# Kernel optimization log

Hardware: AMD Instinct MI355X
Metric: run time of the kernel (lower is better)

Reference implementation:

```python
import jax, jax.numpy as jnp
import numpy as np

POLY_DEGREE = 2
EPS = 1e-10
MAX_INTER = 25

# Upper-triangle index pairs (i<j) in the same row-major order as the
# original double loop: (0,1),(0,2),...,(0,24),(1,2),...
_IU0, _IU1 = np.triu_indices(MAX_INTER, k=1)


def setup_inputs() -> dict:
    key = jax.random.key(0)
    x = jax.random.normal(key, (524288, 25), dtype=jnp.float32)
    return {"x": x}


def reference(x) -> jnp.ndarray:
    feats = [x]
    # polynomial features: degrees 2..POLY_DEGREE
    for degree in range(2, POLY_DEGREE + 1):
        feats.append(jnp.power(x, degree))
    ax = jnp.abs(x) + EPS
    feats.append(jnp.log(ax))            # log features
    feats.append(jnp.sqrt(ax))           # sqrt features
    feats.append(jnp.power(ax, 1.0 / 3.0))  # cbrt features
    # pairwise interactions among first min(F,25) columns, upper triangle
    inter = x[:, _IU0] * x[:, _IU1]      # [B, 300]
    feats.append(inter)
    return jnp.concatenate(feats, axis=1)  # [B, 400]
```

## Files before the change

### kernel.cpp

```cpp
#include <hip/hip_runtime.h>

#define NF    25
#define NPAIR 300
#define NCOL  425
#define ROWS  8
#define BLK   256
#define TILE4 (ROWS * NCOL / 4)

typedef float f32x4 __attribute__((ext_vector_type(4)));

__global__ __launch_bounds__(BLK) void feat_expand_kernel(
    const float* __restrict__ x, float* __restrict__ out,
    int nrows, int nchunks) {
  __shared__ f32x4 tile4[TILE4];
  __shared__ float  xs[ROWS * NF];
  __shared__ unsigned short pairs[NPAIR];
  float* tile = (float*)tile4;

  const int tid = threadIdx.x;

  for (int p = tid; p < NPAIR; p += BLK) {
    int rem = p, i = 0;
    while (rem >= (NF - 1 - i)) { rem -= (NF - 1 - i); ++i; }
    pairs[p] = (unsigned short)(i | ((i + 1 + rem) << 8));
  }

  for (int chunk = blockIdx.x; chunk < nchunks; chunk += gridDim.x) {
    const long long rowbase = (long long)chunk * ROWS;
    const int rows_here = (int)((nrows - rowbase) < ROWS ? (nrows - rowbase) : ROWS);

    __syncthreads();

    if (tid < ROWS * NF) {
      const int r = tid / NF;
      if (r < rows_here) xs[tid] = x[rowbase * NF + tid];
    }
    __syncthreads();

    if (tid < ROWS * NF) {
      const int r = tid / NF, i = tid - r * NF;
      if (r < rows_here) {
        float* tr = &tile[r * NCOL];
        const float v  = xs[tid];
        const float ax = fabsf(v) + 1e-10f;
        const float l2 = __builtin_amdgcn_logf(ax);
        tr[i]          = v;
        tr[NF + i]     = v * v;
        tr[2*NF + i]   = l2 * 0.69314718055994530942f;
        tr[3*NF + i]   = sqrtf(ax);
        tr[4*NF + i]   = __builtin_amdgcn_exp2f(l2 * (1.0f/3.0f));
      }
    }
    for (int p = tid; p < ROWS * NPAIR; p += BLK) {
      const int r = p / NPAIR, q = p - r * NPAIR;
      if (r < rows_here) {
        const unsigned short pr = pairs[q];
        tile[r * NCOL + 5*NF + q] =
            xs[r * NF + (pr & 0xFF)] * xs[r * NF + (pr >> 8)];
      }
    }
    __syncthreads();

    if (rows_here == ROWS) {
      f32x4* __restrict__ o4 = (f32x4*)(out + rowbase * NCOL);
      for (int v = tid; v < TILE4; v += BLK)
        __builtin_nontemporal_store(tile4[v], &o4[v]);
    } else {
      const int total = rows_here * NCOL;
      for (int o = tid; o < total; o += BLK)
        out[rowbase * NCOL + o] = tile[o];
    }
  }
}

extern "C" void kernel_launch(void* const* d_in, const int* in_sizes, int n_in,
                              void* d_out, int out_size, void* d_ws, size_t ws_size,
                              hipStream_t stream) {
  const float* x = (const float*)d_in[0];
  float* out = (float*)d_out;

  const int nrows = in_sizes[0] / NF;
  const int nchunks = (nrows + ROWS - 1) / ROWS;
  const int grid = nchunks < 4096 ? nchunks : 4096;

  feat_expand_kernel<<<grid, BLK, 0, stream>>>(x, out, nrows, nchunks);
}
```

Measured before the change: 212.6 us.

## Prefetch next chunk's input into registers and unroll pair/store loops

Each thread now loads its input element for the next chunk into a register while the current chunk is being computed, which hides global load latency behind the compute and store phases. The pairwise-product and output-store loops are fully unrolled with fixed trip counts, input loads use nontemporal hints, and the grid is capped at 2048 blocks instead of 4096. The kernel is bound by output writes, so the prefetch may add little, and halving the grid reduces the number of blocks in flight.

Result: slower. 227.3 us (+6.9%).

```diff
diff --git a/kernel.cpp b/kernel.cpp
--- a/kernel.cpp
+++ b/kernel.cpp
@@ -5,6 +5,7 @@
 #define NCOL  425
 #define ROWS  8
 #define BLK   256
+#define LOADN (ROWS * NF)
 #define TILE4 (ROWS * NCOL / 4)
 
 typedef float f32x4 __attribute__((ext_vector_type(4)));
@@ -13,11 +14,13 @@
     const float* __restrict__ x, float* __restrict__ out,
     int nrows, int nchunks) {
   __shared__ f32x4 tile4[TILE4];
-  __shared__ float  xs[ROWS * NF];
+  __shared__ float  xs[LOADN];
   __shared__ unsigned short pairs[NPAIR];
   float* tile = (float*)tile4;
 
   const int tid = threadIdx.x;
+  const int r200 = tid / NF;
+  const int i200 = tid - r200 * NF;
 
   for (int p = tid; p < NPAIR; p += BLK) {
     int rem = p, i = 0;
@@ -25,37 +28,53 @@
     pairs[p] = (unsigned short)(i | ((i + 1 + rem) << 8));
   }
 
-  for (int chunk = blockIdx.x; chunk < nchunks; chunk += gridDim.x) {
-    const long long rowbase = (long long)chunk * ROWS;
-    const int rows_here = (int)((nrows - rowbase) < ROWS ? (nrows - rowbase) : ROWS);
+  float v = 0.0f;
+  {
+    const long long c0 = blockIdx.x;
+    if (tid < LOADN && c0 < nchunks) {
+      const long long rowbase = c0 * ROWS;
+      if (rowbase + r200 < nrows)
+        v = __builtin_nontemporal_load(&x[rowbase * NF + tid]);
+    }
+  }
+
+  for (long long chunk = blockIdx.x; chunk < nchunks; chunk += gridDim.x) {
+    const long long rowbase = chunk * ROWS;
+    const long long rem = nrows - rowbase;
+    const int rows_here = (int)(rem < ROWS ? rem : ROWS);
 
     __syncthreads();
-
-    if (tid < ROWS * NF) {
-      const int r = tid / NF;
-      if (r < rows_here) xs[tid] = x[rowbase * NF + tid];
-    }
+    if (tid < LOADN) xs[tid] = v;
     __syncthreads();
 
-    if (tid < ROWS * NF) {
-      const int r = tid / NF, i = tid - r * NF;
-      if (r < rows_here) {
-        float* tr = &tile[r * NCOL];
-        const float v  = xs[tid];
-        const float ax = fabsf(v) + 1e-10f;
-        const float l2 = __builtin_amdgcn_logf(ax);
-        tr[i]          = v;
-        tr[NF + i]     = v * v;
-        tr[2*NF + i]   = l2 * 0.69314718055994530942f;
-        tr[3*NF + i]   = sqrtf(ax);
-        tr[4*NF + i]   = __builtin_amdgcn_exp2f(l2 * (1.0f/3.0f));
+    float vnext = 0.0f;
+    {
+      const long long nc = chunk + gridDim.x;
+      if (tid < LOADN && nc < nchunks) {
+        const long long nbase = nc * ROWS;
+        if (nbase + r200 < nrows)
+          vnext = __builtin_nontemporal_load(&x[nbase * NF + tid]);
       }
     }
-    for (int p = tid; p < ROWS * NPAIR; p += BLK) {
-      const int r = p / NPAIR, q = p - r * NPAIR;
-      if (r < rows_here) {
+
+    if (tid < LOADN) {
+      float* tr = &tile[r200 * NCOL];
+      const float ax = fabsf(v) + 1e-10f;
+      const float l2 = __builtin_amdgcn_logf(ax);
+      tr[i200]        = v;
+      tr[NF + i200]   = v * v;
+      tr[2*NF + i200] = l2 * 0.69314718055994530942f;
+      tr[3*NF + i200] = sqrtf(ax);
+      tr[4*NF + i200] = __builtin_amdgcn_exp2f(l2 * (1.0f/3.0f));
+    }
+
+#pragma unroll
+    for (int k = 0; k < 10; ++k) {
+      const int p = tid + k * BLK;
+      if (k < 9 || p < ROWS * NPAIR) {
+        const int r = p / NPAIR, q = p - r * NPAIR;
         const unsigned short pr = pairs[q];
-        tile[r * NCOL + 5*NF + q] =
+        tile[r * NCOL + 5 * NF + q] =
             xs[r * NF + (pr & 0xFF)] * xs[r * NF + (pr >> 8)];
       }
     }
@@ -63,13 +82,18 @@
 
     if (rows_here == ROWS) {
       f32x4* __restrict__ o4 = (f32x4*)(out + rowbase * NCOL);
-      for (int v = tid; v < TILE4; v += BLK)
-        __builtin_nontemporal_store(tile4[v], &o4[v]);
+      __builtin_nontemporal_store(tile4[tid],            &o4[tid]);
+      __builtin_nontemporal_store(tile4[tid + BLK],      &o4[tid + BLK]);
+      __builtin_nontemporal_store(tile4[tid + 2 * BLK],  &o4[tid + 2 * BLK]);
+      if (tid < TILE4 - 3 * BLK)
+        __builtin_nontemporal_store(tile4[tid + 3 * BLK], &o4[tid + 3 * BLK]);
     } else {
       const int total = rows_here * NCOL;
       for (int o = tid; o < total; o += BLK)
         out[rowbase * NCOL + o] = tile[o];
     }
+
+    v = vnext;
   }
 }
 
@@ -81,7 +105,7 @@
 
   const int nrows = in_sizes[0] / NF;
   const int nchunks = (nrows + ROWS - 1) / ROWS;
-  const int grid = nchunks < 4096 ? nchunks : 4096;
+  const int grid = nchunks < 2048 ? nchunks : 2048;
 
   feat_expand_kernel<<<grid, BLK, 0, stream>>>(x, out, nrows, nchunks);
 }
```

## Compute pairwise products directly in store loop via precomputed index table

Applied to the files above, without the earlier changes.

Drops the staged output tile. Each block now precomputes a per-output-dword table of two LDS indices, and the store loop gathers and multiplies values on the fly, with unary features multiplied by a constant 1.0 slot. This removes one barrier and the tile write and reread round trip, and the x load goes straight to registers. In exchange it adds a table read plus two scalar LDS gathers per output element, which may cause bank conflicts.

Measured after the change: 214.7 us. Within noise of the previous version (+1.0%).

```diff
diff --git a/kernel.cpp b/kernel.cpp
--- a/kernel.cpp
+++ b/kernel.cpp
@@ -1,74 +1,89 @@
 #include <hip/hip_runtime.h>
 
-#define NF    25
-#define NPAIR 300
-#define NCOL  425
-#define ROWS  8
-#define BLK   256
-#define TILE4 (ROWS * NCOL / 4)
+#define NF     25
+#define NPAIR  300
+#define NUNARY 125
+#define NCOL   425
+#define ROWS   8
+#define BLK    256
+#define TILE_DW (ROWS * NCOL)
+#define TILE4   (TILE_DW / 4)
+#define VALS_N  (ROWS * NF + ROWS * NUNARY + 4)
 
 typedef float f32x4 __attribute__((ext_vector_type(4)));
+typedef unsigned int u32;
+typedef u32 u32x4 __attribute__((ext_vector_type(4)));
+
+#define ONE_SLOT (ROWS * NF + ROWS * NUNARY)
 
 __global__ __launch_bounds__(BLK) void feat_expand_kernel(
     const float* __restrict__ x, float* __restrict__ out,
     int nrows, int nchunks) {
-  __shared__ f32x4 tile4[TILE4];
-  __shared__ float  xs[ROWS * NF];
-  __shared__ unsigned short pairs[NPAIR];
-  float* tile = (float*)tile4;
+  __shared__ float vals[VALS_N];
+  __shared__ u32x4 dtab4[TILE4];
+  u32* dtab = (u32*)dtab4;
 
   const int tid = threadIdx.x;
+  const int r200 = tid / NF;
+  const int i200 = tid - r200 * NF;
 
-  for (int p = tid; p < NPAIR; p += BLK) {
-    int rem = p, i = 0;
-    while (rem >= (NF - 1 - i)) { rem -= (NF - 1 - i); ++i; }
-    pairs[p] = (unsigned short)(i | ((i + 1 + rem) << 8));
+  if (tid == 0) vals[ONE_SLOT] = 1.0f;
+  for (int o = tid; o < TILE_DW; o += BLK) {
+    const int r = o / NCOL, c = o - r * NCOL;
+    u32 d;
+    if (c < NUNARY) {
+      d = (u32)(ROWS * NF + r * NUNARY + c) | ((u32)ONE_SLOT << 16);
+    } else {
+      int rem = c - NUNARY, i = 0;
+      while (rem >= (NF - 1 - i)) { rem -= (NF - 1 - i); ++i; }
+      const int j = i + 1 + rem;
+      d = (u32)(r * NF + i) | ((u32)(r * NF + j) << 16);
+    }
+    dtab[o] = d;
   }
 
   for (int chunk = blockIdx.x; chunk < nchunks; chunk += gridDim.x) {
     const long long rowbase = (long long)chunk * ROWS;
-    const int rows_here = (int)((nrows - rowbase) < ROWS ? (nrows - rowbase) : ROWS);
+    const long long remrows = nrows - rowbase;
+    const int rows_here = (int)(remrows < ROWS ? remrows : ROWS);
 
     __syncthreads();
 
-    if (tid < ROWS * NF) {
-      const int r = tid / NF;
-      if (r < rows_here) xs[tid] = x[rowbase * NF + tid];
-    }
-    __syncthreads();
-
-    if (tid < ROWS * NF) {
-      const int r = tid / NF, i = tid - r * NF;
-      if (r < rows_here) {
-        float* tr = &tile[r * NCOL];
-        const float v  = xs[tid];
-        const float ax = fabsf(v) + 1e-10f;
-        const float l2 = __builtin_amdgcn_logf(ax);
-        tr[i]          = v;
-        tr[NF + i]     = v * v;
-        tr[2*NF + i]   = l2 * 0.69314718055994530942f;
-        tr[3*NF + i]   = sqrtf(ax);
-        tr[4*NF + i]   = __builtin_amdgcn_exp2f(l2 * (1.0f/3.0f));
-      }
-    }
-    for (int p = tid; p < ROWS * NPAIR; p += BLK) {
-      const int r = p / NPAIR, q = p - r * NPAIR;
-      if (r < rows_here) {
-        const unsigned short pr = pairs[q];
-        tile[r * NCOL + 5*NF + q] =
-            xs[r * NF + (pr & 0xFF)] * xs[r * NF + (pr >> 8)];
-      }
+    if (tid < ROWS * NF && r200 < rows_here) {
+      const float v = x[rowbase * NF + tid];
+      vals[tid] = v;
+      float* ur = &vals[ROWS * NF + r200 * NUNARY];
+      const float ax = fabsf(v) + 1e-10f;
+      const float l2 = __builtin_amdgcn_logf(ax);
+      ur[i200]          = v;
+      ur[NF + i200]     = v * v;
+      ur[2*NF + i200]   = l2 * 0.69314718055994530942f;
+      ur[3*NF + i200]   = sqrtf(ax);
+      ur[4*NF + i200]   = __builtin_amdgcn_exp2f(l2 * (1.0f/3.0f));
     }
     __syncthreads();
 
     if (rows_here == ROWS) {
       f32x4* __restrict__ o4 = (f32x4*)(out + rowbase * NCOL);
-      for (int v = tid; v < TILE4; v += BLK)
-        __builtin_nontemporal_store(tile4[v], &o4[v]);
+#pragma unroll
+      for (int k = 0; k < 4; ++k) {
+        const int v4 = tid + k * BLK;
+        if (k < 3 || v4 < TILE4) {
+          const u32x4 d = dtab4[v4];
+          f32x4 ov;
+          ov.x = vals[d.x & 0xFFFF] * vals[d.x >> 16];
+          ov.y = vals[d.y & 0xFFFF] * vals[d.y >> 16];
+          ov.z = vals[d.z & 0xFFFF] * vals[d.z >> 16];
+          ov.w = vals[d.w & 0xFFFF] * vals[d.w >> 16];
+          __builtin_nontemporal_store(ov, &o4[v4]);
+        }
+      }
     } else {
       const int total = rows_here * NCOL;
-      for (int o = tid; o < total; o += BLK)
-        out[rowbase * NCOL + o] = tile[o];
+      for (int o = tid; o < total; o += BLK) {
+        const u32 d = dtab[o];
+        out[rowbase * NCOL + o] = vals[d & 0xFFFF] * vals[d >> 16];
+      }
     }
   }
 }
```
